# Kernel optimization log

Hardware: AMD Instinct MI355X
Metric: run time of the kernel (lower is better)

## Reference

```python
import jax, jax.numpy as jnp
import numpy as np
from jax import lax


def fps_indices(xyz, n_points):
    """Farthest point sampling. xyz: [B, N, 3]. Returns int32 indices [B, n_points].

    Classic PointNet++ algorithm: start from point 0, maintain per-point running
    min squared distance to the selected set, pick argmax each iteration.
    """
    B, N, _ = xyz.shape

    def step(carry, _):
        min_d, last_idx = carry  # min_d: [B, N], last_idx: [B]
        last_pt = jnp.take_along_axis(xyz, last_idx[:, None, None], axis=1)  # [B,1,3]
        d = jnp.sum((xyz - last_pt) ** 2, axis=-1)  # [B, N] squared dist to last pick
        min_d = jnp.minimum(min_d, d)
        nxt = jnp.argmax(min_d, axis=-1).astype(jnp.int32)  # [B]
        return (min_d, nxt), last_idx

    init = (jnp.full((B, N), jnp.inf, dtype=xyz.dtype), jnp.zeros((B,), jnp.int32))
    _, idxs = lax.scan(step, init, None, length=n_points)  # [n_points, B]
    return idxs.T  # [B, n_points]


def setup_inputs() -> dict:
    key = jax.random.key(0)
    k1, k2 = jax.random.split(key)
    B, C, N = 16, 128, 16384
    x = jax.random.normal(k1, (B, C, N), dtype=jnp.float32)
    x_xyz = jax.random.normal(k2, (B, 3, N), dtype=jnp.float32)
    return {"x": x, "x_xyz": x_xyz, "n_points": 4096}


def reference(x, x_xyz, n_points):
    # x: [B, C, N] features, x_xyz: [B, 3, N] coordinates (channels-first)
    xyz = jnp.transpose(x_xyz, (0, 2, 1))  # [B, N, 3]
    idx = fps_indices(xyz, n_points)  # [B, S] int32
    # Gather features and coordinates at sampled indices (channels-first output)
    x_s = jnp.take_along_axis(x, idx[:, None, :], axis=2)        # [B, C, S]
    xyz_s = jnp.take_along_axis(x_xyz, idx[:, None, :], axis=2)  # [B, 3, S]
    return x_s, xyz_s
```

## Files before the change

kernel.cpp:

```cpp
#include <hip/hip_runtime.h>
#include <hip/hip_bf16.h>

#pragma clang fp contract(off)

#define NTH   1024
#define PPT   16
#define NPTS  16384
#define BATCH 16
#define CFEAT 128
#define SMAX  4096
#define NWAVE (NTH / 64)
#define PRUNE_C 0.999995f

__device__ __forceinline__ unsigned spread3(unsigned v) {
    v &= 0x3FFu;
    v = (v | (v << 16)) & 0x030000FFu;
    v = (v | (v << 8))  & 0x0300F00Fu;
    v = (v | (v << 4))  & 0x030C30C3u;
    v = (v | (v << 2))  & 0x09249249u;
    return v;
}
__device__ __forceinline__ unsigned qz10(float v) {
    int q = (int)((v + 6.0f) * (1023.0f / 12.0f));
    q = q < 0 ? 0 : (q > 1023 ? 1023 : q);
    return (unsigned)q;
}
__device__ __forceinline__ unsigned morton30(float x, float y, float z) {
    return (spread3(qz10(x)) << 2) | (spread3(qz10(y)) << 1) | spread3(qz10(z));
}

template <bool FUSED>
__global__ __launch_bounds__(NTH) void fps_kernel(const float* __restrict__ xyz,
                                                  const float* __restrict__ x,
                                                  int* __restrict__ idx_out,
                                                  float* __restrict__ out,
                                                  int S) {
    const int b    = blockIdx.x;
    const int tid  = threadIdx.x;
    const int wid  = tid >> 6;
    const int lane = tid & 63;
    const float* __restrict__ xb = xyz + (size_t)b * 3 * NPTS;

    __shared__ unsigned s_ord[NPTS];
    __shared__ unsigned s_hist[256];
    __shared__ unsigned long long s_slot[4];
    __shared__ int s_idx[SMAX];

    for (int i = tid; i < 256; i += NTH) s_hist[i] = 0;
    __syncthreads();
    for (int k = 0; k < PPT; ++k) {
        const int p = k * NTH + tid;
        const unsigned m = morton30(xb[p], xb[NPTS + p], xb[2 * NPTS + p]);
        atomicAdd(&s_hist[m >> 22], 1u);
    }
    __syncthreads();
    if (tid == 0) {
        unsigned acc = 0;
        for (int i = 0; i < 256; ++i) { const unsigned c = s_hist[i]; s_hist[i] = acc; acc += c; }
    }
    __syncthreads();
    for (int k = 0; k < PPT; ++k) {
        const int p = k * NTH + tid;
        const unsigned m = morton30(xb[p], xb[NPTS + p], xb[2 * NPTS + p]);
        const unsigned pos = atomicAdd(&s_hist[m >> 22], 1u);
        s_ord[pos] = (unsigned)p;
    }
    if (tid == 0) { s_slot[0] = s_slot[1] = s_slot[2] = s_slot[3] = 0ull; }
    __syncthreads();

    float X[PPT], Y[PPT], Z[PPT], D[PPT];
    unsigned VI[PPT / 2];
    float bxl =  INFINITY, byl =  INFINITY, bzl =  INFINITY;
    float bxh = -INFINITY, byh = -INFINITY, bzh = -INFINITY;
#pragma unroll
    for (int k = 0; k < PPT; ++k) {
        const unsigned gi = s_ord[wid * (64 * PPT) + k * 64 + lane];
        const float xx = xb[gi], yy = xb[NPTS + gi], zz = xb[2 * NPTS + gi];
        X[k] = xx; Y[k] = yy; Z[k] = zz; D[k] = INFINITY;
        if ((k & 1) == 0) VI[k >> 1] = gi;
        else              VI[k >> 1] |= (gi << 16);
        bxl = fminf(bxl, xx); bxh = fmaxf(bxh, xx);
        byl = fminf(byl, yy); byh = fmaxf(byh, yy);
        bzl = fminf(bzl, zz); bzh = fmaxf(bzh, zz);
    }
#pragma unroll
    for (int off = 32; off >= 1; off >>= 1) {
        bxl = fminf(bxl, __shfl_xor(bxl, off)); bxh = fmaxf(bxh, __shfl_xor(bxh, off));
        byl = fminf(byl, __shfl_xor(byl, off)); byh = fmaxf(byh, __shfl_xor(byh, off));
        bzl = fminf(bzl, __shfl_xor(bzl, off)); bzh = fmaxf(bzh, __shfl_xor(bzh, off));
    }

    int   last  = 0;
    float px = xb[0], py = xb[NPTS], pz = xb[2 * NPTS];
    float wBest = INFINITY;
    unsigned long long myPack = 0;

    for (int t = 0; t < S; ++t) {
        if (tid == 0) s_idx[t] = last;

        const float gx = fmaxf(fmaxf(bxl - px, px - bxh), 0.0f);
        const float gy = fmaxf(fmaxf(byl - py, py - byh), 0.0f);
        const float gz = fmaxf(fmaxf(bzl - pz, pz - bzh), 0.0f);
        const float lb = gx * gx + gy * gy + gz * gz;

        if (!(lb * PRUNE_C >= wBest)) {
            float bestv = -INFINITY;
#pragma unroll
            for (int k = 0; k < PPT; ++k) {
                const float dx = X[k] - px, dy = Y[k] - py, dz = Z[k] - pz;
                const float d  = __builtin_fmaf(dz, dz, __builtin_fmaf(dx, dx, dy * dy));
                const float md = fminf(D[k], d);
                D[k] = md;
                bestv = fmaxf(bestv, md);
            }
            const unsigned mybits = __float_as_uint(bestv);

            unsigned red = mybits;
#define DPP_MAX_STEP(CTRL)                                                     \
            {                                                                  \
                const unsigned tpp = (unsigned)__builtin_amdgcn_update_dpp(    \
                    0, (int)red, (CTRL), 0xf, 0xf, true);                      \
                red = (tpp > red) ? tpp : red;                                 \
            }
            DPP_MAX_STEP(0x111)
            DPP_MAX_STEP(0x112)
            DPP_MAX_STEP(0x114)
            DPP_MAX_STEP(0x118)
            DPP_MAX_STEP(0x142)
            DPP_MAX_STEP(0x143)
#undef DPP_MAX_STEP
            const unsigned bu = (unsigned)__builtin_amdgcn_readlane((int)red, 63);
            wBest = __uint_as_float(bu);

            myPack = 0;
            if (mybits == bu) {
                unsigned mo = 0xFFFFFFFFu;
#pragma unroll
                for (int k = 0; k < PPT; ++k) {
                    if (__float_as_uint(D[k]) == mybits) {
                        const unsigned gg = (VI[k >> 1] >> ((k & 1) * 16)) & 0xFFFFu;
                        mo = (gg < mo) ? gg : mo;
                    }
                }
                myPack = ((unsigned long long)mybits << 32)
                       | (unsigned long long)(0xFFFFFFFFu - mo);
            }
        }
        if (myPack) atomicMax(&s_slot[t & 3], myPack);
        if (tid == 0) s_slot[(t + 2) & 3] = 0ull;
        __syncthreads();

        const unsigned long long win = s_slot[t & 3];
        last = (int)(0xFFFFFFFFu - (unsigned)(win & 0xFFFFFFFFull));
        px = xb[last]; py = xb[NPTS + last]; pz = xb[2 * NPTS + last];
    }

    __syncthreads();
    if (!FUSED) {
        for (int i = tid; i < S; i += NTH) idx_out[b * S + i] = s_idx[i];
    } else {
        for (int i = tid; i < CFEAT * S; i += NTH) {
            const int c = i / S, s = i - c * S;
            const long r = (long)b * CFEAT + c;
            out[r * S + s] = x[r * NPTS + s_idx[s]];
        }
        const long base2 = (long)BATCH * CFEAT * S;
        for (int i = tid; i < 3 * S; i += NTH) {
            const int c = i / S, s = i - c * S;
            const long r = (long)b * 3 + c;
            out[base2 + r * S + s] = xyz[r * NPTS + s_idx[s]];
        }
    }
}

__global__ void gather_kernel(const float* __restrict__ x,
                              const float* __restrict__ xyz,
                              const int* __restrict__ idx,
                              float* __restrict__ out,
                              int S) {
    const long nxs   = (long)BATCH * CFEAT * S;
    const long total = nxs + (long)BATCH * 3 * S;
    for (long i = (long)blockIdx.x * blockDim.x + threadIdx.x; i < total;
         i += (long)gridDim.x * blockDim.x) {
        if (i < nxs) {
            const int s  = (int)(i % S);
            const long r = i / S;
            const int b  = (int)(r / CFEAT);
            const int p  = idx[b * S + s];
            out[i] = x[r * NPTS + p];
        } else {
            const long j = i - nxs;
            const int s  = (int)(j % S);
            const long r = j / S;
            const int b  = (int)(r / 3);
            const int p  = idx[b * S + s];
            out[i] = xyz[r * NPTS + p];
        }
    }
}

extern "C" void kernel_launch(void* const* d_in, const int* in_sizes, int n_in,
                              void* d_out, int out_size, void* d_ws, size_t ws_size,
                              hipStream_t stream) {
    const float* x   = nullptr;
    const float* xyz = nullptr;
    for (int i = 0; i < n_in; ++i) {
        if (in_sizes[i] == BATCH * CFEAT * NPTS)  x   = (const float*)d_in[i];
        else if (in_sizes[i] == BATCH * 3 * NPTS) xyz = (const float*)d_in[i];
    }
    float* out = (float*)d_out;
    const int S = out_size / (BATCH * (CFEAT + 3));

    const size_t need = (size_t)BATCH * (size_t)S * sizeof(int);
    if (ws_size >= need && d_ws != nullptr) {
        int* idx = (int*)d_ws;
        fps_kernel<false><<<BATCH, NTH, 0, stream>>>(xyz, nullptr, idx, nullptr, S);
        gather_kernel<<<2048, 256, 0, stream>>>(x, xyz, idx, out, S);
    } else {
        fps_kernel<true><<<BATCH, NTH, 0, stream>>>(xyz, x, nullptr, out, S);
    }
}
```

Measured before the change: 4.491 ms.

## Replace shared atomicMax with per-wave slots and broadcast winner coordinates via LDS

Each FPS iteration now has one owner lane per wave write a packed (distance, index) key and that point's coordinates into a double-buffered per-wave LDS slot, replacing the shared 64-bit atomicMax. After the barrier every thread scans the 16 wave slots to find the winner. The next query point's coordinates are read from LDS rather than from global memory, taking a dependent global load off the serial critical path. Waves whose bounding box is pruned copy their previous slot forward, and the owner lane is picked by ballot plus a min-shuffle on ties. The cost is a 16-entry LDS scan per thread per iteration.

New measurement: 7.216 ms. 1.61x slower.

```diff
diff --git a/kernel.cpp b/kernel.cpp
--- a/kernel.cpp
+++ b/kernel.cpp
@@ -43,8 +43,9 @@
 
     __shared__ unsigned s_ord[NPTS];
     __shared__ unsigned s_hist[256];
-    __shared__ unsigned long long s_slot[4];
-    __shared__ int s_idx[SMAX];
+    __shared__ unsigned long long s_wpk[2][NWAVE];
+    __shared__ float    s_cx[2][NWAVE], s_cy[2][NWAVE], s_cz[2][NWAVE];
+    __shared__ int      s_idx[SMAX];
 
     for (int i = tid; i < 256; i += NTH) s_hist[i] = 0;
     __syncthreads();
@@ -65,7 +66,6 @@
         const unsigned pos = atomicAdd(&s_hist[m >> 22], 1u);
         s_ord[pos] = (unsigned)p;
     }
-    if (tid == 0) { s_slot[0] = s_slot[1] = s_slot[2] = s_slot[3] = 0ull; }
     __syncthreads();
 
     float X[PPT], Y[PPT], Z[PPT], D[PPT];
@@ -93,10 +93,10 @@
     int   last  = 0;
     float px = xb[0], py = xb[NPTS], pz = xb[2 * NPTS];
     float wBest = INFINITY;
-    unsigned long long myPack = 0;
 
     for (int t = 0; t < S; ++t) {
         if (tid == 0) s_idx[t] = last;
+        const int buf = t & 1;
 
         const float gx = fmaxf(fmaxf(bxl - px, px - bxh), 0.0f);
         const float gy = fmaxf(fmaxf(byl - py, py - byh), 0.0f);
@@ -132,27 +132,57 @@
             const unsigned bu = (unsigned)__builtin_amdgcn_readlane((int)red, 63);
             wBest = __uint_as_float(bu);
 
-            myPack = 0;
-            if (mybits == bu) {
-                unsigned mo = 0xFFFFFFFFu;
-#pragma unroll
-                for (int k = 0; k < PPT; ++k) {
+            unsigned mo = 0xFFFFFFFFu;
+            float cx = 0.f, cy = 0.f, cz = 0.f;
+            const bool cand = (mybits == bu);
+            if (cand) {
+#pragma unroll
+                for (int k = PPT - 1; k >= 0; --k) {
                     if (__float_as_uint(D[k]) == mybits) {
-                        const unsigned gg = (VI[k >> 1] >> ((k & 1) * 16)) & 0xFFFFu;
-                        mo = (gg < mo) ? gg : mo;
+                        mo = (VI[k >> 1] >> ((k & 1) * 16)) & 0xFFFFu;
+                        cx = X[k]; cy = Y[k]; cz = Z[k];
                     }
                 }
-                myPack = ((unsigned long long)mybits << 32)
-                       | (unsigned long long)(0xFFFFFFFFu - mo);
-            }
-        }
-        if (myPack) atomicMax(&s_slot[t & 3], myPack);
-        if (tid == 0) s_slot[(t + 2) & 3] = 0ull;
+            }
+            const unsigned long long m = __ballot(cand);
+            bool owner = cand;
+            if (__popcll(m) > 1) {
+                unsigned mn = mo;
+#pragma unroll
+                for (int off = 32; off >= 1; off >>= 1) {
+                    const unsigned o = __shfl_xor(mn, off);
+                    mn = (o < mn) ? o : mn;
+                }
+                owner = cand && (mo == mn);
+            }
+            if (owner) {
+                s_wpk[buf][wid] = ((unsigned long long)bu << 32)
+                                | (unsigned long long)(0xFFFFFFFFu - mo);
+                s_cx[buf][wid] = cx;
+                s_cy[buf][wid] = cy;
+                s_cz[buf][wid] = cz;
+            }
+        } else {
+            if (lane == 0) {
+                s_wpk[buf][wid] = s_wpk[buf ^ 1][wid];
+                s_cx[buf][wid] = s_cx[buf ^ 1][wid];
+                s_cy[buf][wid] = s_cy[buf ^ 1][wid];
+                s_cz[buf][wid] = s_cz[buf ^ 1][wid];
+            }
+        }
         __syncthreads();
 
-        const unsigned long long win = s_slot[t & 3];
+        unsigned long long win = s_wpk[buf][0];
+        int w = 0;
+#pragma unroll
+        for (int w2 = 1; w2 < NWAVE; ++w2) {
+            const unsigned long long pw = s_wpk[buf][w2];
+            if (pw > win) { win = pw; w = w2; }
+        }
         last = (int)(0xFFFFFFFFu - (unsigned)(win & 0xFFFFFFFFull));
-        px = xb[last]; py = xb[NPTS + last]; pz = xb[2 * NPTS + last];
+        px = s_cx[buf][w];
+        py = s_cy[buf][w];
+        pz = s_cz[buf][w];
     }
 
     __syncthreads();
```
